# Performance work log

Measured on AMD Instinct MI355X. Metric: run time of the kernel, lower is better.

Reference implementation:

```python
import jax, jax.numpy as jnp
import numpy as np

# Granite-8B-like dims
B, S, H = 4, 1024, 4096
NH, NKV, D = 32, 8, 128          # query heads, kv heads (GQA), head_dim
PG, NPAGES = 128, 64             # page_size, pool size
PPS = S // PG                    # pages per sequence = 8
SCALE = 0.08838834764831845      # attention_multiplier (1/sqrt(128))
SOFTCAP = 50.0                   # attention_logit_softcapping


def rotate_half(x):
    x1, x2 = jnp.split(x, 2, axis=-1)
    return jnp.concatenate([-x2, x1], axis=-1)


def setup_inputs() -> dict:
    key = jax.random.key(0)
    ks = jax.random.split(key, 5)
    hidden_states = jax.random.normal(ks[0], (B, S, H), jnp.float32)
    wq = jax.random.normal(ks[1], (H, NH * D), jnp.float32) * 0.02
    wk = jax.random.normal(ks[2], (H, NKV * D), jnp.float32) * 0.02
    wv = jax.random.normal(ks[3], (H, NKV * D), jnp.float32) * 0.02
    wo = jax.random.normal(ks[4], (NH * D, H), jnp.float32) * 0.02
    # RoPE tables (HF convention), position_ids = arange(S)
    inv_freq = 1.0 / (10000.0 ** (jnp.arange(0, D, 2, dtype=jnp.float32) / D))
    freqs = jnp.outer(jnp.arange(S, dtype=jnp.float32), inv_freq)  # [S, D/2]
    emb = jnp.concatenate([freqs, freqs], axis=-1)                 # [S, D]
    cos, sin = jnp.cos(emb), jnp.sin(emb)
    # Disjoint random physical pages per sequence (page-table indirection)
    perm = np.random.default_rng(0).permutation(NPAGES)[: B * PPS]
    page_table = jnp.asarray(perm.reshape(B, PPS), jnp.int32)      # [B, PPS]
    return dict(hidden_states=hidden_states, wq=wq, wk=wk, wv=wv, wo=wo,
                cos=cos, sin=sin, page_table=page_table)


def reference(hidden_states, wq, wk, wv, wo, cos, sin, page_table):
    Bb, Ss, _ = hidden_states.shape
    # projections + head split: [B, nH, S, D]
    q = (hidden_states @ wq).reshape(Bb, Ss, NH, D).transpose(0, 2, 1, 3)
    k = (hidden_states @ wk).reshape(Bb, Ss, NKV, D).transpose(0, 2, 1, 3)
    v = (hidden_states @ wv).reshape(Bb, Ss, NKV, D).transpose(0, 2, 1, 3)
    # RoPE (cos/sin broadcast over batch and heads)
    q = q * cos + rotate_half(q) * sin
    k = k * cos + rotate_half(k) * sin
    # physical slot for each (b, s): page_table[b, s//PG]*PG + s%PG
    s_idx = jnp.arange(Ss)
    phys = page_table[:, s_idx // PG] * PG + (s_idx % PG)           # [B, S]
    N = NPAGES * PG
    # scatter K/V into the shared paged cache (pages are disjoint across B)
    k_flat = k.transpose(1, 0, 2, 3).reshape(NKV, Bb * Ss, D)
    v_flat = v.transpose(1, 0, 2, 3).reshape(NKV, Bb * Ss, D)
    flat = phys.reshape(-1)
    k_cache = jnp.zeros((NKV, N, D), hidden_states.dtype).at[:, flat, :].set(k_flat)
    v_cache = jnp.zeros((NKV, N, D), hidden_states.dtype).at[:, flat, :].set(v_flat)
    # gather back in logical order per sequence: [B, NKV, S, D]
    k_log = k_cache[:, phys, :].transpose(1, 0, 2, 3)
    v_log = v_cache[:, phys, :].transpose(1, 0, 2, 3)
    # GQA: expand kv heads to query heads
    g = NH // NKV
    kr = jnp.repeat(k_log, g, axis=1)
    vr = jnp.repeat(v_log, g, axis=1)
    # scaled QK -> softcap -> causal mask (score_mod order) -> softmax
    scores = jnp.einsum('bhqd,bhkd->bhqk', q, kr) * SCALE
    scores = SOFTCAP * jnp.tanh(scores / SOFTCAP)
    causal = jnp.tril(jnp.ones((Ss, Ss), bool))
    scores = jnp.where(causal, scores, jnp.finfo(scores.dtype).min)
    p = jax.nn.softmax(scores, axis=-1)
    out = jnp.einsum('bhqk,bhkd->bhqd', p, vr)
    out = out.transpose(0, 2, 1, 3).reshape(Bb, Ss, NH * D)
    return out @ wo
```

## Files before the change

kernel.cpp:

```cpp
#include <hip/hip_runtime.h>
#include <hip/hip_bf16.h>


#define S_    1024
#define NQKV  6144
#define SCALE_   0.08838834764831845f
#define SOFTCAP_ 50.0f

typedef __bf16 bf16x8 __attribute__((ext_vector_type(8)));
typedef float  f32x4  __attribute__((ext_vector_type(4)));
typedef unsigned int  u32;
typedef unsigned short u16;

static __device__ __forceinline__ u16 f2bf(float f) {
  union { float f; u32 u; } v; v.f = f;
  u32 u = v.u;
  u32 r = u + 0x7FFFu + ((u >> 16) & 1u);
  return (u16)(r >> 16);
}
static __device__ __forceinline__ float bf2f(u16 s) {
  union { u32 u; float f; } v; v.u = ((u32)s) << 16; return v.f;
}

static __device__ __forceinline__ void gload_lds16(const void* g, void* l) {
  __builtin_amdgcn_global_load_lds(
      (const __attribute__((address_space(1))) void*)g,
      (__attribute__((address_space(3))) void*)l, 16, 0, 0);
}

__global__ __launch_bounds__(256) void cast_bf16(const float* __restrict__ X,
                                                 u16* __restrict__ Y) {
  size_t i = (size_t)blockIdx.x * 256 + threadIdx.x;
  float4 a = ((const float4*)X)[2 * i];
  float4 b = ((const float4*)X)[2 * i + 1];
  union { u16 h[8]; f32x4 v; } o;
  o.h[0] = f2bf(a.x); o.h[1] = f2bf(a.y); o.h[2] = f2bf(a.z); o.h[3] = f2bf(a.w);
  o.h[4] = f2bf(b.x); o.h[5] = f2bf(b.y); o.h[6] = f2bf(b.z); o.h[7] = f2bf(b.w);
  ((f32x4*)Y)[i] = o.v;
}

__global__ __launch_bounds__(256) void transpose_w(const float* __restrict__ W,
                                                   u16* __restrict__ WT, int N) {
  __shared__ float t[32][33];
  const int K = 4096;
  int n0 = blockIdx.x * 32, k0 = blockIdx.y * 32;
  int tx = threadIdx.x & 31, ty = threadIdx.x >> 5;
#pragma unroll
  for (int j = 0; j < 4; ++j)
    t[ty + 8 * j][tx] = W[(size_t)(k0 + ty + 8 * j) * N + n0 + tx];
  __syncthreads();
#pragma unroll
  for (int j = 0; j < 4; ++j)
    WT[(size_t)(n0 + ty + 8 * j) * K + k0 + tx] = f2bf(t[tx][ty + 8 * j]);
}

template <bool OUT_BF16>
__global__ __launch_bounds__(256) void gemm_mfma(const u16* __restrict__ A,
                                                 const u16* __restrict__ Bt,
                                                 void* __restrict__ Cp,
                                                 int N, int K) {
  __shared__ u16 As[128 * 32];
  __shared__ u16 Bs[128 * 32];
  int tid = threadIdx.x;
  int wave = tid >> 6, lane = tid & 63;
  int quad = lane >> 4, l16 = lane & 15;
  int wrow = (wave >> 1) * 64, wcol = (wave & 1) * 64;
  int m0 = blockIdx.y * 128, n0 = blockIdx.x * 128;

  f32x4 acc[4][4];
#pragma unroll
  for (int i = 0; i < 4; ++i)
#pragma unroll
    for (int j = 0; j < 4; ++j)
#pragma unroll
      for (int c = 0; c < 4; ++c) acc[i][j][c] = 0.0f;

  int lr = lane >> 2, lc = lane & 3;
  const u16* ga = A  + (size_t)(m0 + wave * 32 + lr) * K + lc * 8;
  const u16* gb = Bt + (size_t)(n0 + wave * 32 + lr) * K + lc * 8;
  u16* lA0 = &As[(wave * 32) * 32];
  u16* lA1 = &As[(wave * 32 + 16) * 32];
  u16* lB0 = &Bs[(wave * 32) * 32];
  u16* lB1 = &Bs[(wave * 32 + 16) * 32];
  const size_t rstep = (size_t)16 * K;

  for (int k0 = 0; k0 < K; k0 += 32) {
    gload_lds16(ga + k0,         lA0);
    gload_lds16(ga + rstep + k0, lA1);
    gload_lds16(gb + k0,         lB0);
    gload_lds16(gb + rstep + k0, lB1);
    __syncthreads();
    bf16x8 af[4], bfr[4];
#pragma unroll
    for (int fi = 0; fi < 4; ++fi) {
      af[fi]  = *(const bf16x8*)&As[(wrow + fi * 16 + l16) * 32 + quad * 8];
      bfr[fi] = *(const bf16x8*)&Bs[(wcol + fi * 16 + l16) * 32 + quad * 8];
    }
#pragma unroll
    for (int mf = 0; mf < 4; ++mf)
#pragma unroll
      for (int nf = 0; nf < 4; ++nf)
        acc[mf][nf] = __builtin_amdgcn_mfma_f32_16x16x32_bf16(
            af[mf], bfr[nf], acc[mf][nf], 0, 0, 0);
    __syncthreads();
  }
#pragma unroll
  for (int mf = 0; mf < 4; ++mf)
#pragma unroll
    for (int nf = 0; nf < 4; ++nf)
#pragma unroll
      for (int r = 0; r < 4; ++r) {
        int row = m0 + wrow + mf * 16 + quad * 4 + r;
        int col = n0 + wcol + nf * 16 + l16;
        float v = acc[mf][nf][r];
        if (OUT_BF16) ((u16*)Cp)[(size_t)row * N + col] = f2bf(v);
        else          ((float*)Cp)[(size_t)row * N + col] = v;
      }
}

__global__ __launch_bounds__(256) void rope_kernel(u16* __restrict__ QKV,
                                                   const float* __restrict__ cosT,
                                                   const float* __restrict__ sinT) {
  int row = blockIdx.x;
  int s = row & (S_ - 1);
  u32* Q32 = (u32*)(QKV + (size_t)row * NQKV);
  const float2* c2 = (const float2*)(cosT + s * 128);
  const float2* s2 = (const float2*)(sinT + s * 128);
#pragma unroll
  for (int i = 0; i < 5; ++i) {
    int e = threadIdx.x + 256 * i;
    int head = e >> 5, dd = e & 31;
    int col2 = head * 64 + dd;
    u32 a = Q32[col2];
    u32 b = Q32[col2 + 32];
    float2 c = c2[dd], sn = s2[dd];
    float x1a = bf2f((u16)a), x1b = bf2f((u16)(a >> 16));
    float x2a = bf2f((u16)b), x2b = bf2f((u16)(b >> 16));
    Q32[col2]      = (u32)f2bf(x1a * c.x - x2a * sn.x) |
                     ((u32)f2bf(x1b * c.y - x2b * sn.y) << 16);
    Q32[col2 + 32] = (u32)f2bf(x2a * c.x + x1a * sn.x) |
                     ((u32)f2bf(x2b * c.y + x1b * sn.y) << 16);
  }
}

__global__ __launch_bounds__(256) void attn_kernel(const u16* __restrict__ QKV,
                                                   u16* __restrict__ ctx) {
  __shared__ __align__(16) u16 ks[64 * 128];
  __shared__ __align__(16) u16 vT[128 * 64];
  __shared__ __align__(16) u16 ps[4][16 * 64];
  int bx = blockIdx.x;
  int qt = bx & 15, h = (bx >> 4) & 31, b = bx >> 9;
  int kvh = h >> 2;
  int tid = threadIdx.x, wave = tid >> 6, lane = tid & 63;
  int quad = lane >> 4, l16 = lane & 15;
  int q0 = qt * 64 + wave * 16;

  bf16x8 qf[4];
  {
    const u16* qrow = QKV + (size_t)(b * S_ + q0 + l16) * NQKV + h * 128;
#pragma unroll
    for (int k4 = 0; k4 < 4; ++k4)
      qf[k4] = *(const bf16x8*)(qrow + k4 * 32 + quad * 8);
  }
  f32x4 acc[8];
#pragma unroll
  for (int i = 0; i < 8; ++i)
#pragma unroll
    for (int r = 0; r < 4; ++r) acc[i][r] = 0.0f;
  float m[4], l[4];
#pragma unroll
  for (int r = 0; r < 4; ++r) { m[r] = -3e30f; l[r] = 0.f; }

  const u16* kbase = QKV + (size_t)(b * S_) * NQKV + 4096 + kvh * 128;
  const u32* vbase = (const u32*)(QKV + (size_t)(b * S_) * NQKV + 5120 + kvh * 128);

  int krow = tid >> 4, kc16 = tid & 15;
  int klo = lane & 1, A = (lane >> 1) & 3, D = (lane >> 3) & 7;
  int vkey0 = 2 * A + klo;

  f32x4 kreg[4];
  u32 vreg[16];

  auto LOADK = [&](int cc) {
#pragma unroll
    for (int i = 0; i < 4; ++i)
      kreg[i] = *(const f32x4*)(kbase +
                 (size_t)(cc * 64 + krow + 16 * i) * NQKV + kc16 * 8);
  };
  auto LOADV = [&](int cc) {
#pragma unroll
    for (int i = 0; i < 16; ++i) {
      int key = (wave * 2 + (i >> 3)) * 8 + vkey0;
      int dp  = (i & 7) * 8 + D;
      vreg[i] = vbase[(size_t)(cc * 64 + key) * (NQKV / 2) + dp];
    }
  };
  auto WRITEK = [&]() {
#pragma unroll
    for (int i = 0; i < 4; ++i) {
      int r = krow + 16 * i;
      u32 off = (u32)(r * 256 + kc16 * 16) ^ (u32)((r & 7) << 4);
      *(f32x4*)((char*)ks + off) = kreg[i];
    }
  };
  auto WRITEV = [&]() {
#pragma unroll
    for (int i = 0; i < 16; ++i) {
      u32 v = vreg[i];
      u32 vo = __shfl_xor(v, 1, 64);
      u32 w = klo ? ((vo >> 16) | (v & 0xFFFF0000u))
                  : ((v & 0xFFFFu) | (vo << 16));
      int dp = (i & 7) * 8 + D;
      int d = 2 * dp + klo;
      int kp = (wave * 2 + (i >> 3)) * 4 + A;
      u32 off = (u32)(d * 128 + kp * 4) ^ (u32)((d & 7) << 4);
      *(u32*)((char*)vT + off) = w;
    }
  };

  LOADK(0); LOADV(0);
  WRITEK(); WRITEV();
  __syncthreads();

  for (int c = 0; c <= qt; ++c) {
    if (c < qt) { LOADK(c + 1); LOADV(c + 1); }

    f32x4 s[4];
    __builtin_amdgcn_s_setprio(1);
#pragma unroll
    for (int nf = 0; nf < 4; ++nf) {
#pragma unroll
      for (int r = 0; r < 4; ++r) s[nf][r] = 0.0f;
      int row = l16 + 16 * nf;
#pragma unroll
      for (int k4 = 0; k4 < 4; ++k4) {
        u32 off = (u32)(row * 256 + k4 * 64 + quad * 16) ^ (u32)((row & 7) << 4);
        bf16x8 kf = *(const bf16x8*)((const char*)ks + off);
        s[nf] = __builtin_amdgcn_mfma_f32_16x16x32_bf16(qf[k4], kf, s[nf], 0, 0, 0);
      }
    }
    __builtin_amdgcn_s_setprio(0);

#pragma unroll
    for (int r = 0; r < 4; ++r) {
      float sc[4];
#pragma unroll
      for (int nf = 0; nf < 4; ++nf) {
        float x = s[nf][r] * SCALE_;
        float e2 = __expf(x * (2.0f / SOFTCAP_));
        sc[nf] = SOFTCAP_ * (1.0f - 2.0f / (e2 + 1.0f));
      }
      if (c == qt) {
        int row = wave * 16 + quad * 4 + r;
#pragma unroll
        for (int nf = 0; nf < 4; ++nf)
          if (nf * 16 + l16 > row) sc[nf] = -1e30f;
      }
      float cm = fmaxf(fmaxf(sc[0], sc[1]), fmaxf(sc[2], sc[3]));
#pragma unroll
      for (int off = 8; off >= 1; off >>= 1)
        cm = fmaxf(cm, __shfl_xor(cm, off, 64));
      float mn = fmaxf(m[r], cm);
      float alpha = __expf(m[r] - mn);
      float p[4], psum = 0.f;
#pragma unroll
      for (int nf = 0; nf < 4; ++nf) { p[nf] = __expf(sc[nf] - mn); psum += p[nf]; }
#pragma unroll
      for (int off = 8; off >= 1; off >>= 1) psum += __shfl_xor(psum, off, 64);
      l[r] = l[r] * alpha + psum;
      m[r] = mn;
#pragma unroll
      for (int i = 0; i < 8; ++i) acc[i][r] *= alpha;
      int prow = quad * 4 + r;
#pragma unroll
      for (int nf = 0; nf < 4; ++nf) {
        u32 off = (u32)(prow * 128 + (nf * 16 + l16) * 2) ^ (u32)((prow & 7) << 4);
        *(u16*)((char*)&ps[wave][0] + off) = f2bf(p[nf]);
      }
    }
    bf16x8 pa[2];
#pragma unroll
    for (int k2 = 0; k2 < 2; ++k2) {
      u32 off = (u32)(l16 * 128 + k2 * 64 + quad * 16) ^ (u32)((l16 & 7) << 4);
      pa[k2] = *(const bf16x8*)((const char*)&ps[wave][0] + off);
    }
    __builtin_amdgcn_s_setprio(1);
#pragma unroll
    for (int nf = 0; nf < 8; ++nf) {
      int d = l16 + 16 * nf;
#pragma unroll
      for (int k2 = 0; k2 < 2; ++k2) {
        u32 off = (u32)(d * 128 + k2 * 64 + quad * 16) ^ (u32)((d & 7) << 4);
        bf16x8 vf = *(const bf16x8*)((const char*)vT + off);
        acc[nf] = __builtin_amdgcn_mfma_f32_16x16x32_bf16(pa[k2], vf, acc[nf], 0, 0, 0);
      }
    }
    __builtin_amdgcn_s_setprio(0);

    __syncthreads();
    if (c < qt) {
      WRITEK(); WRITEV();
      __syncthreads();
    }
  }
#pragma unroll
  for (int r = 0; r < 4; ++r) {
    float inv = 1.0f / l[r];
    size_t rowoff = (size_t)(b * S_ + q0 + quad * 4 + r) * 4096 + h * 128;
#pragma unroll
    for (int nf = 0; nf < 8; ++nf)
      ctx[rowoff + nf * 16 + l16] = f2bf(acc[nf][r] * inv);
  }
}

extern "C" void kernel_launch(void* const* d_in, const int* in_sizes, int n_in,
                              void* d_out, int out_size, void* d_ws, size_t ws_size,
                              hipStream_t stream) {
  (void)in_sizes; (void)n_in; (void)out_size; (void)ws_size;
  const float* hidden = (const float*)d_in[0];
  const float* wq = (const float*)d_in[1];
  const float* wk = (const float*)d_in[2];
  const float* wv = (const float*)d_in[3];
  const float* wo = (const float*)d_in[4];
  const float* cosT = (const float*)d_in[5];
  const float* sinT = (const float*)d_in[6];

  u16* WT  = (u16*)d_ws;
  u16* QKV = WT + (size_t)10240 * 4096;
  u16* CTX = WT;
  u16* Hbf = (u16*)d_out;

  transpose_w<<<dim3(4096 / 32, 128), 256, 0, stream>>>(wq, WT, 4096);
  transpose_w<<<dim3(1024 / 32, 128), 256, 0, stream>>>(wk, WT + (size_t)4096 * 4096, 1024);
  transpose_w<<<dim3(1024 / 32, 128), 256, 0, stream>>>(wv, WT + (size_t)5120 * 4096, 1024);
  transpose_w<<<dim3(4096 / 32, 128), 256, 0, stream>>>(wo, WT + (size_t)6144 * 4096, 4096);
  cast_bf16<<<8192, 256, 0, stream>>>(hidden, Hbf);

  gemm_mfma<true><<<dim3(6144 / 128, 4096 / 128), 256, 0, stream>>>(
      Hbf, WT, QKV, 6144, 4096);
  rope_kernel<<<4096, 256, 0, stream>>>(QKV, cosT, sinT);
  attn_kernel<<<2048, 256, 0, stream>>>(QKV, CTX);
  gemm_mfma<false><<<dim3(4096 / 128, 4096 / 128), 256, 0, stream>>>(
      CTX, WT + (size_t)6144 * 4096, d_out, 4096, 4096);
}
```

Before: 995.2 us.

## Pair causal query tiles per block and use fixed-offset softmax via softcap bound

Each attention block now processes two query tiles (15-ii and ii) so causal work is balanced across a half-size grid. Because softcapping bounds logits to ±50, the online max tracking and accumulator rescaling are replaced by a fixed exponent offset, with tanh folded into the exp argument. The row sum is reduced across lanes once at the end. This removes per-chunk shuffles and rescales, at the cost of relying on the softcap bound for numerical range and fewer blocks for occupancy.

```diff
diff --git a/kernel.cpp b/kernel.cpp
--- a/kernel.cpp
+++ b/kernel.cpp
@@ -149,27 +149,10 @@
   __shared__ __align__(16) u16 vT[128 * 64];
   __shared__ __align__(16) u16 ps[4][16 * 64];
   int bx = blockIdx.x;
-  int qt = bx & 15, h = (bx >> 4) & 31, b = bx >> 9;
+  int ii = bx & 7, h = (bx >> 3) & 31, b = bx >> 8;
   int kvh = h >> 2;
   int tid = threadIdx.x, wave = tid >> 6, lane = tid & 63;
   int quad = lane >> 4, l16 = lane & 15;
-  int q0 = qt * 64 + wave * 16;
-
-  bf16x8 qf[4];
-  {
-    const u16* qrow = QKV + (size_t)(b * S_ + q0 + l16) * NQKV + h * 128;
-#pragma unroll
-    for (int k4 = 0; k4 < 4; ++k4)
-      qf[k4] = *(const bf16x8*)(qrow + k4 * 32 + quad * 8);
-  }
-  f32x4 acc[8];
-#pragma unroll
-  for (int i = 0; i < 8; ++i)
-#pragma unroll
-    for (int r = 0; r < 4; ++r) acc[i][r] = 0.0f;
-  float m[4], l[4];
-#pragma unroll
-  for (int r = 0; r < 4; ++r) { m[r] = -3e30f; l[r] = 0.f; }
 
   const u16* kbase = QKV + (size_t)(b * S_) * NQKV + 4096 + kvh * 128;
   const u32* vbase = (const u32*)(QKV + (size_t)(b * S_) * NQKV + 5120 + kvh * 128);
@@ -218,98 +201,106 @@
     }
   };
 
-  LOADK(0); LOADV(0);
-  WRITEK(); WRITEV();
-  __syncthreads();
-
-  for (int c = 0; c <= qt; ++c) {
-    if (c < qt) { LOADK(c + 1); LOADV(c + 1); }
-
-    f32x4 s[4];
-    __builtin_amdgcn_s_setprio(1);
-#pragma unroll
-    for (int nf = 0; nf < 4; ++nf) {
-#pragma unroll
-      for (int r = 0; r < 4; ++r) s[nf][r] = 0.0f;
-      int row = l16 + 16 * nf;
-#pragma unroll
-      for (int k4 = 0; k4 < 4; ++k4) {
-        u32 off = (u32)(row * 256 + k4 * 64 + quad * 16) ^ (u32)((row & 7) << 4);
-        bf16x8 kf = *(const bf16x8*)((const char*)ks + off);
-        s[nf] = __builtin_amdgcn_mfma_f32_16x16x32_bf16(qf[k4], kf, s[nf], 0, 0, 0);
-      }
-    }
-    __builtin_amdgcn_s_setprio(0);
-
+#pragma unroll 1
+  for (int pass = 0; pass < 2; ++pass) {
+    int qt = pass ? ii : 15 - ii;
+    int q0 = qt * 64 + wave * 16;
+
+    bf16x8 qf[4];
+    {
+      const u16* qrow = QKV + (size_t)(b * S_ + q0 + l16) * NQKV + h * 128;
+#pragma unroll
+      for (int k4 = 0; k4 < 4; ++k4)
+        qf[k4] = *(const bf16x8*)(qrow + k4 * 32 + quad * 8);
+    }
+    f32x4 acc[8];
+#pragma unroll
+    for (int i = 0; i < 8; ++i)
+#pragma unroll
+      for (int r = 0; r < 4; ++r) acc[i][r] = 0.0f;
+    float lp[4] = {0.f, 0.f, 0.f, 0.f};
+
+    LOADK(0); LOADV(0);
+    WRITEK(); WRITEV();
+    __syncthreads();
+
+    for (int c = 0; c <= qt; ++c) {
+      if (c < qt) { LOADK(c + 1); LOADV(c + 1); }
+
+      f32x4 s[4];
+      __builtin_amdgcn_s_setprio(1);
+#pragma unroll
+      for (int nf = 0; nf < 4; ++nf) {
+#pragma unroll
+        for (int r = 0; r < 4; ++r) s[nf][r] = 0.0f;
+        int row = l16 + 16 * nf;
+#pragma unroll
+        for (int k4 = 0; k4 < 4; ++k4) {
+          u32 off = (u32)(row * 256 + k4 * 64 + quad * 16) ^ (u32)((row & 7) << 4);
+          bf16x8 kf = *(const bf16x8*)((const char*)ks + off);
+          s[nf] = __builtin_amdgcn_mfma_f32_16x16x32_bf16(qf[k4], kf, s[nf], 0, 0, 0);
+        }
+      }
+      __builtin_amdgcn_s_setprio(0);
+
+#pragma unroll
+      for (int r = 0; r < 4; ++r) {
+        float p[4];
+#pragma unroll
+        for (int nf = 0; nf < 4; ++nf) {
+          float e2 = __expf(s[nf][r] * (SCALE_ / 25.0f));
+          p[nf] = __expf(38.0f - 100.0f / (e2 + 1.0f));
+        }
+        if (c == qt) {
+          int row = wave * 16 + quad * 4 + r;
+#pragma unroll
+          for (int nf = 0; nf < 4; ++nf)
+            if (nf * 16 + l16 > row) p[nf] = 0.0f;
+        }
+        lp[r] += (p[0] + p[1]) + (p[2] + p[3]);
+        int prow = quad * 4 + r;
+#pragma unroll
+        for (int nf = 0; nf < 4; ++nf) {
+          u32 off = (u32)(prow * 128 + (nf * 16 + l16) * 2) ^ (u32)((prow & 7) << 4);
+          *(u16*)((char*)&ps[wave][0] + off) = f2bf(p[nf]);
+        }
+      }
+      bf16x8 pa[2];
+#pragma unroll
+      for (int k2 = 0; k2 < 2; ++k2) {
+        u32 off = (u32)(l16 * 128 + k2 * 64 + quad * 16) ^ (u32)((l16 & 7) << 4);
+        pa[k2] = *(const bf16x8*)((const char*)&ps[wave][0] + off);
+      }
+      __builtin_amdgcn_s_setprio(1);
+#pragma unroll
+      for (int nf = 0; nf < 8; ++nf) {
+        int d = l16 + 16 * nf;
+#pragma unroll
+        for (int k2 = 0; k2 < 2; ++k2) {
+          u32 off = (u32)(d * 128 + k2 * 64 + quad * 16) ^ (u32)((d & 7) << 4);
+          bf16x8 vf = *(const bf16x8*)((const char*)vT + off);
+          acc[nf] = __builtin_amdgcn_mfma_f32_16x16x32_bf16(pa[k2], vf, acc[nf], 0, 0, 0);
+        }
+      }
+      __builtin_amdgcn_s_setprio(0);
+
+      __syncthreads();
+      if (c < qt) {
+        WRITEK(); WRITEV();
+        __syncthreads();
+      }
+    }
 #pragma unroll
     for (int r = 0; r < 4; ++r) {
-      float sc[4];
-#pragma unroll
-      for (int nf = 0; nf < 4; ++nf) {
-        float x = s[nf][r] * SCALE_;
-        float e2 = __expf(x * (2.0f / SOFTCAP_));
-        sc[nf] = SOFTCAP_ * (1.0f - 2.0f / (e2 + 1.0f));
-      }
-      if (c == qt) {
-        int row = wave * 16 + quad * 4 + r;
-#pragma unroll
-        for (int nf = 0; nf < 4; ++nf)
-          if (nf * 16 + l16 > row) sc[nf] = -1e30f;
-      }
-      float cm = fmaxf(fmaxf(sc[0], sc[1]), fmaxf(sc[2], sc[3]));
-#pragma unroll
-      for (int off = 8; off >= 1; off >>= 1)
-        cm = fmaxf(cm, __shfl_xor(cm, off, 64));
-      float mn = fmaxf(m[r], cm);
-      float alpha = __expf(m[r] - mn);
-      float p[4], psum = 0.f;
-#pragma unroll
-      for (int nf = 0; nf < 4; ++nf) { p[nf] = __expf(sc[nf] - mn); psum += p[nf]; }
-#pragma unroll
-      for (int off = 8; off >= 1; off >>= 1) psum += __shfl_xor(psum, off, 64);
-      l[r] = l[r] * alpha + psum;
-      m[r] = mn;
-#pragma unroll
-      for (int i = 0; i < 8; ++i) acc[i][r] *= alpha;
-      int prow = quad * 4 + r;
-#pragma unroll
-      for (int nf = 0; nf < 4; ++nf) {
-        u32 off = (u32)(prow * 128 + (nf * 16 + l16) * 2) ^ (u32)((prow & 7) << 4);
-        *(u16*)((char*)&ps[wave][0] + off) = f2bf(p[nf]);
-      }
-    }
-    bf16x8 pa[2];
-#pragma unroll
-    for (int k2 = 0; k2 < 2; ++k2) {
-      u32 off = (u32)(l16 * 128 + k2 * 64 + quad * 16) ^ (u32)((l16 & 7) << 4);
-      pa[k2] = *(const bf16x8*)((const char*)&ps[wave][0] + off);
-    }
-    __builtin_amdgcn_s_setprio(1);
-#pragma unroll
-    for (int nf = 0; nf < 8; ++nf) {
-      int d = l16 + 16 * nf;
-#pragma unroll
-      for (int k2 = 0; k2 < 2; ++k2) {
-        u32 off = (u32)(d * 128 + k2 * 64 + quad * 16) ^ (u32)((d & 7) << 4);
-        bf16x8 vf = *(const bf16x8*)((const char*)vT + off);
-        acc[nf] = __builtin_amdgcn_mfma_f32_16x16x32_bf16(pa[k2], vf, acc[nf], 0, 0, 0);
-      }
-    }
-    __builtin_amdgcn_s_setprio(0);
-
-    __syncthreads();
-    if (c < qt) {
-      WRITEK(); WRITEV();
-      __syncthreads();
-    }
-  }
-#pragma unroll
-  for (int r = 0; r < 4; ++r) {
-    float inv = 1.0f / l[r];
-    size_t rowoff = (size_t)(b * S_ + q0 + quad * 4 + r) * 4096 + h * 128;
-#pragma unroll
-    for (int nf = 0; nf < 8; ++nf)
-      ctx[rowoff + nf * 16 + l16] = f2bf(acc[nf][r] * inv);
+      float ls = lp[r];
+#pragma unroll
+      for (int off = 8; off >= 1; off >>= 1) ls += __shfl_xor(ls, off, 64);
+      float inv = 1.0f / ls;
+      size_t rowoff = (size_t)(b * S_ + q0 + quad * 4 + r) * 4096 + h * 128;
+#pragma unroll
+      for (int nf = 0; nf < 8; ++nf)
+        ctx[rowoff + nf * 16 + l16] = f2bf(acc[nf][r] * inv);
+    }
   }
 }
 
@@ -339,7 +330,7 @@
   gemm_mfma<true><<<dim3(6144 / 128, 4096 / 128), 256, 0, stream>>>(
       Hbf, WT, QKV, 6144, 4096);
   rope_kernel<<<4096, 256, 0, stream>>>(QKV, cosT, sinT);
-  attn_kernel<<<2048, 256, 0, stream>>>(QKV, CTX);
+  attn_kernel<<<1024, 256, 0, stream>>>(QKV, CTX);
   gemm_mfma<false><<<dim3(4096 / 128, 4096 / 128), 256, 0, stream>>>(
       CTX, WT + (size_t)6144 * 4096, d_out, 4096, 4096);
 }
```

After: 971.9 us. 2.3% less time.
